# Kernel tuning notes

Measured on AMD Instinct MI355X. Metric: run time of the kernel, lower is better.

Reference implementation:

```python
import jax, jax.numpy as jnp
import numpy as np

ALPHA = 0.2  # LeakyReLU negative slope
NEG_INF = -9e15  # mask value used by the torch dense GAT layer

def _gat_layer(x, adj, W, a1, a2):
    # x: [N, F], W: [F, Fh], a1/a2: [Fh]
    Wh = x @ W                                   # [N, Fh]
    f1 = Wh @ a1                                 # [N] source scores
    f2 = Wh @ a2                                 # [N] dest scores
    e = jax.nn.leaky_relu(f1[:, None] + f2[None, :], ALPHA)  # [N, N]
    att = jnp.where(adj > 0, e, NEG_INF)
    att = jax.nn.softmax(att, axis=1)
    return att @ Wh                              # [N, Fh]

def setup_inputs():
    key = jax.random.key(0)
    ks = jax.random.split(key, 8)
    N, F, H, Fh, C = 6144, 512, 4, 64, 40
    x = jax.random.normal(ks[0], (N, F), jnp.float32)
    # sparse-ish binary adjacency with self loops (dense storage as in the module)
    adj = (jax.random.uniform(ks[1], (N, N)) < 0.005).astype(jnp.float32)
    adj = jnp.maximum(adj, jnp.eye(N, dtype=jnp.float32))
    s = 1.0 / np.sqrt(Fh)
    W = jax.random.normal(ks[2], (H, F, Fh), jnp.float32) * s
    a1 = jax.random.normal(ks[3], (H, Fh), jnp.float32) * s
    a2 = jax.random.normal(ks[4], (H, Fh), jnp.float32) * s
    so = 1.0 / np.sqrt(C)
    Wo = jax.random.normal(ks[5], (H * Fh, C), jnp.float32) * so
    ao1 = jax.random.normal(ks[6], (C,), jnp.float32) * so
    ao2 = jax.random.normal(ks[7], (C,), jnp.float32) * so
    return {"x": x, "adj": adj, "W": W, "a1": a1, "a2": a2,
            "Wo": Wo, "ao1": ao1, "ao2": ao2}

def reference(x, adj, W, a1, a2, Wo, ao1, ao2):
    N = x.shape[0]
    # multi-head layer (concat=True -> ELU applied inside each head)
    heads = jax.vmap(_gat_layer, in_axes=(None, None, 0, 0, 0))(x, adj, W, a1, a2)  # [H, N, Fh]
    h = jax.nn.elu(heads)
    h = jnp.transpose(h, (1, 0, 2)).reshape(N, -1)   # concat heads -> [N, H*Fh]
    # output attention layer (concat=False), then outer ELU from GAT.forward
    out = jax.nn.elu(_gat_layer(h, adj, Wo, ao1, ao2))  # [N, C]
    return jax.nn.log_softmax(out, axis=1)
```

## Files before the change

### kernel.cpp

```cpp
#include <hip/hip_runtime.h>
#include <stdint.h>

#define N_NODES 6144
#define F_IN 512
#define NHEAD 4
#define FH 64
#define HF 256
#define NCLS 40
#define NCLSP 48
#define CAP 192
#define LRELU_ALPHA 0.2f

typedef __bf16 bf16x8 __attribute__((ext_vector_type(8)));
typedef float floatx4 __attribute__((ext_vector_type(4)));

__device__ __forceinline__ float b2f(uint16_t u){
    union { float f; uint32_t i; } x; x.i = ((uint32_t)u) << 16; return x.f;
}
__device__ __forceinline__ uint16_t f2b(float f){
    union { float f; uint32_t i; } x; x.f = f;
    uint32_t r = x.i + 0x7FFFu + ((x.i >> 16) & 1u);
    return (uint16_t)(r >> 16);
}


__global__ void k_prep(const float* __restrict__ x, const float* __restrict__ W,
                       const float* __restrict__ Wo,
                       uint16_t* __restrict__ xh, uint16_t* __restrict__ xl,
                       uint16_t* __restrict__ Wth, uint16_t* __restrict__ Wtl,
                       uint16_t* __restrict__ Woth, uint16_t* __restrict__ Wotl){
    int b = blockIdx.x, t = threadIdx.x;
    if (b < 1536){
        int T = b * 256 + t;
        int n = T >> 6, q8 = T & 63;
        const float4* xp = reinterpret_cast<const float4*>(x + (size_t)n * F_IN + q8 * 8);
        float4 v0 = xp[0], v1 = xp[1];
        int rt = n >> 4, m = n & 15, kc = q8 >> 2, q = q8 & 3;
        size_t off = ((size_t)(rt * 16 + kc) << 9) + (q * 16 + m) * 8;
        ushort4 h0, h1, l0, l1;
        h0.x = f2b(v0.x); l0.x = f2b(v0.x - b2f(h0.x));
        h0.y = f2b(v0.y); l0.y = f2b(v0.y - b2f(h0.y));
        h0.z = f2b(v0.z); l0.z = f2b(v0.z - b2f(h0.z));
        h0.w = f2b(v0.w); l0.w = f2b(v0.w - b2f(h0.w));
        h1.x = f2b(v1.x); l1.x = f2b(v1.x - b2f(h1.x));
        h1.y = f2b(v1.y); l1.y = f2b(v1.y - b2f(h1.y));
        h1.z = f2b(v1.z); l1.z = f2b(v1.z - b2f(h1.z));
        h1.w = f2b(v1.w); l1.w = f2b(v1.w - b2f(h1.w));
        *reinterpret_cast<ushort4*>(xh + off)     = h0;
        *reinterpret_cast<ushort4*>(xh + off + 4) = h1;
        *reinterpret_cast<ushort4*>(xl + off)     = l0;
        *reinterpret_cast<ushort4*>(xl + off + 4) = l1;
    } else if (b < 1600){
        int T = (b - 1536) * 256 + t;
        int c = T >> 6, q8 = T & 63;
        int h = c >> 6, f = c & 63, k0 = q8 * 8;
        int rt = c >> 4, m = c & 15, kc = q8 >> 2, q = q8 & 3;
        size_t off = ((size_t)(rt * 16 + kc) << 9) + (q * 16 + m) * 8;
        #pragma unroll
        for (int j = 0; j < 8; j++){
            float v = W[h * 32768 + (k0 + j) * 64 + f];
            uint16_t hi = f2b(v);
            Wth[off + j] = hi;
            Wtl[off + j] = f2b(v - b2f(hi));
        }
    } else {
        int T = (b - 1600) * 256 + t;
        int c = T >> 8, k = T & 255;
        float v = (c < NCLS) ? Wo[k * NCLS + c] : 0.f;
        uint16_t hi = f2b(v);
        Woth[c * HF + k] = hi;
        Wotl[c * HF + k] = f2b(v - b2f(hi));
    }
}

__global__ void k_build_csr(const float* __restrict__ adj, int* __restrict__ cnt,
                            int* __restrict__ idxbuf){
    __shared__ int scnt;
    int i = blockIdx.x, t = threadIdx.x;
    if (t == 0) scnt = 0;
    __syncthreads();
    const float4* row = reinterpret_cast<const float4*>(adj + (size_t)i * N_NODES);
    int* out = idxbuf + (size_t)i * CAP;
    for (int q = t; q < N_NODES / 4; q += 256){
        float4 v = row[q];
        int j0 = q * 4;
        if (v.x != 0.f){ int p = atomicAdd(&scnt, 1); if (p < CAP) out[p] = j0;     }
        if (v.y != 0.f){ int p = atomicAdd(&scnt, 1); if (p < CAP) out[p] = j0 + 1; }
        if (v.z != 0.f){ int p = atomicAdd(&scnt, 1); if (p < CAP) out[p] = j0 + 2; }
        if (v.w != 0.f){ int p = atomicAdd(&scnt, 1); if (p < CAP) out[p] = j0 + 3; }
    }
    __syncthreads();
    if (t == 0) cnt[i] = scnt < CAP ? scnt : CAP;
}

__global__ void k_gemm1(const uint16_t* __restrict__ xh, const uint16_t* __restrict__ xl,
                        const uint16_t* __restrict__ Wth, const uint16_t* __restrict__ Wtl,
                        float* __restrict__ Wh1){
    int w = threadIdx.x >> 6, l = threadIdx.x & 63;
    int rt0 = blockIdx.x * 4 + (w & 1) * 2;
    int ct0 = blockIdx.y * 4 + (w >> 1) * 2;
    const uint16_t* pah = xh  + ((size_t)rt0 << 13) + l * 8;
    const uint16_t* pal = xl  + ((size_t)rt0 << 13) + l * 8;
    const uint16_t* pbh = Wth + ((size_t)ct0 << 13) + l * 8;
    const uint16_t* pbl = Wtl + ((size_t)ct0 << 13) + l * 8;
    floatx4 acc[2][2] = {};
    for (int kc = 0; kc < 16; kc++){
        int o0 = kc * 512, o1 = kc * 512 + 8192;
        bf16x8 a0h = *reinterpret_cast<const bf16x8*>(pah + o0);
        bf16x8 a0l = *reinterpret_cast<const bf16x8*>(pal + o0);
        bf16x8 a1h = *reinterpret_cast<const bf16x8*>(pah + o1);
        bf16x8 a1l = *reinterpret_cast<const bf16x8*>(pal + o1);
        bf16x8 b0h = *reinterpret_cast<const bf16x8*>(pbh + o0);
        bf16x8 b0l = *reinterpret_cast<const bf16x8*>(pbl + o0);
        bf16x8 b1h = *reinterpret_cast<const bf16x8*>(pbh + o1);
        bf16x8 b1l = *reinterpret_cast<const bf16x8*>(pbl + o1);
        acc[0][0] = __builtin_amdgcn_mfma_f32_16x16x32_bf16(a0h, b0l, acc[0][0], 0, 0, 0);
        acc[0][0] = __builtin_amdgcn_mfma_f32_16x16x32_bf16(a0l, b0h, acc[0][0], 0, 0, 0);
        acc[0][0] = __builtin_amdgcn_mfma_f32_16x16x32_bf16(a0h, b0h, acc[0][0], 0, 0, 0);
        acc[0][1] = __builtin_amdgcn_mfma_f32_16x16x32_bf16(a0h, b1l, acc[0][1], 0, 0, 0);
        acc[0][1] = __builtin_amdgcn_mfma_f32_16x16x32_bf16(a0l, b1h, acc[0][1], 0, 0, 0);
        acc[0][1] = __builtin_amdgcn_mfma_f32_16x16x32_bf16(a0h, b1h, acc[0][1], 0, 0, 0);
        acc[1][0] = __builtin_amdgcn_mfma_f32_16x16x32_bf16(a1h, b0l, acc[1][0], 0, 0, 0);
        acc[1][0] = __builtin_amdgcn_mfma_f32_16x16x32_bf16(a1l, b0h, acc[1][0], 0, 0, 0);
        acc[1][0] = __builtin_amdgcn_mfma_f32_16x16x32_bf16(a1h, b0h, acc[1][0], 0, 0, 0);
        acc[1][1] = __builtin_amdgcn_mfma_f32_16x16x32_bf16(a1h, b1l, acc[1][1], 0, 0, 0);
        acc[1][1] = __builtin_amdgcn_mfma_f32_16x16x32_bf16(a1l, b1h, acc[1][1], 0, 0, 0);
        acc[1][1] = __builtin_amdgcn_mfma_f32_16x16x32_bf16(a1h, b1h, acc[1][1], 0, 0, 0);
    }
    int m = l & 15, q = l >> 4;
    #pragma unroll
    for (int fr = 0; fr < 2; fr++){
        #pragma unroll
        for (int fc = 0; fc < 2; fc++){
            int col  = (ct0 + fc) * 16 + m;
            int rowb = (rt0 + fr) * 16 + q * 4;
            #pragma unroll
            for (int r = 0; r < 4; r++)
                Wh1[(size_t)(rowb + r) * HF + col] = acc[fr][fc][r];
        }
    }
}

__global__ void k_f12(const float* __restrict__ Wh1, const float* __restrict__ a1,
                      const float* __restrict__ a2, float* __restrict__ f1,
                      float* __restrict__ f2){
    int n = blockIdx.x;
    int h = threadIdx.x >> 6, l = threadIdx.x & 63;
    float w = Wh1[(size_t)n * HF + h * FH + l];
    float s1 = w * a1[h * FH + l];
    float s2 = w * a2[h * FH + l];
    for (int off = 32; off; off >>= 1){
        s1 += __shfl_xor(s1, off);
        s2 += __shfl_xor(s2, off);
    }
    if (l == 0){ f1[h * N_NODES + n] = s1; f2[h * N_NODES + n] = s2; }
}

__global__ void k_attn1(const int* __restrict__ cnt, const int* __restrict__ idxbuf,
                        const float* __restrict__ Wh1, const float* __restrict__ f1,
                        const float* __restrict__ f2,
                        uint16_t* __restrict__ hch, uint16_t* __restrict__ hcl){
    int i = blockIdx.x, h = threadIdx.x >> 6, l = threadIdx.x & 63;
    int c = cnt[i];
    __shared__ int   sidx[CAP];
    __shared__ float sp[NHEAD][CAP];
    const int* src = idxbuf + (size_t)i * CAP;
    for (int e = threadIdx.x; e < c; e += 256) sidx[e] = src[e];
    __syncthreads();
    float f1i = f1[h * N_NODES + i];
    const float* f2h = f2 + h * N_NODES;
    float mx = -1e30f;
    for (int e = l; e < c; e += 64){
        float s = f1i + f2h[sidx[e]];
        s = s > 0.f ? s : LRELU_ALPHA * s;
        sp[h][e] = s;
        mx = fmaxf(mx, s);
    }
    for (int off = 32; off; off >>= 1) mx = fmaxf(mx, __shfl_xor(mx, off));
    float ssum = 0.f;
    for (int e = l; e < c; e += 64){
        float p = __expf(sp[h][e] - mx);
        sp[h][e] = p;
        ssum += p;
    }
    for (int off = 32; off; off >>= 1) ssum += __shfl_xor(ssum, off);
    float inv = 1.f / ssum;
    float acc = 0.f;
    const float* whb = Wh1 + h * FH + l;
    int e = 0;
    for (; e + 4 <= c; e += 4){
        int j0 = sidx[e], j1 = sidx[e+1], j2 = sidx[e+2], j3 = sidx[e+3];
        float v0 = whb[(size_t)j0 * HF];
        float v1 = whb[(size_t)j1 * HF];
        float v2 = whb[(size_t)j2 * HF];
        float v3 = whb[(size_t)j3 * HF];
        acc += sp[h][e]*v0 + sp[h][e+1]*v1 + sp[h][e+2]*v2 + sp[h][e+3]*v3;
    }
    for (; e < c; e++)
        acc += sp[h][e] * whb[(size_t)sidx[e] * HF];
    acc *= inv;
    float v = acc > 0.f ? acc : __expf(acc) - 1.f;
    uint16_t hi = f2b(v);
    uint16_t lo = f2b(v - b2f(hi));
    size_t o = (size_t)i * HF + h * FH + l;
    hch[o] = hi;
    hcl[o] = lo;
}

__global__ void k_gemm2(const uint16_t* __restrict__ hch, const uint16_t* __restrict__ hcl,
                        const uint16_t* __restrict__ Woth, const uint16_t* __restrict__ Wotl,
                        float* __restrict__ Wh2){
    int w = threadIdx.x >> 6, l = threadIdx.x & 63;
    int r0 = blockIdx.x * 32 + w * 16;
    int c0 = blockIdx.y * 16;
    int m = l & 15, q = l >> 4;
    const uint16_t* pah = hch  + (size_t)(r0 + m) * HF + q * 8;
    const uint16_t* pal = hcl  + (size_t)(r0 + m) * HF + q * 8;
    const uint16_t* pbh = Woth + (size_t)(c0 + m) * HF + q * 8;
    const uint16_t* pbl = Wotl + (size_t)(c0 + m) * HF + q * 8;
    floatx4 acc = {};
    for (int k0 = 0; k0 < HF; k0 += 32){
        bf16x8 ah = *reinterpret_cast<const bf16x8*>(pah + k0);
        bf16x8 al = *reinterpret_cast<const bf16x8*>(pal + k0);
        bf16x8 bh = *reinterpret_cast<const bf16x8*>(pbh + k0);
        bf16x8 bl = *reinterpret_cast<const bf16x8*>(pbl + k0);
        acc = __builtin_amdgcn_mfma_f32_16x16x32_bf16(ah, bl, acc, 0, 0, 0);
        acc = __builtin_amdgcn_mfma_f32_16x16x32_bf16(al, bh, acc, 0, 0, 0);
        acc = __builtin_amdgcn_mfma_f32_16x16x32_bf16(ah, bh, acc, 0, 0, 0);
    }
    int col = c0 + m;
    if (col < NCLS){
        int rowb = r0 + q * 4;
        #pragma unroll
        for (int r = 0; r < 4; r++)
            Wh2[(size_t)(rowb + r) * NCLS + col] = acc[r];
    }
}

__global__ void k_f12o(const float* __restrict__ Wh2, const float* __restrict__ ao1,
                       const float* __restrict__ ao2, float* __restrict__ f1o,
                       float* __restrict__ f2o){
    int w = threadIdx.x >> 6, l = threadIdx.x & 63;
    int n = blockIdx.x * 4 + w;
    float t1 = 0.f, t2 = 0.f;
    if (l < NCLS){
        float v = Wh2[(size_t)n * NCLS + l];
        t1 = v * ao1[l];
        t2 = v * ao2[l];
    }
    for (int off = 32; off; off >>= 1){
        t1 += __shfl_xor(t1, off);
        t2 += __shfl_xor(t2, off);
    }
    if (l == 0){ f1o[n] = t1; f2o[n] = t2; }
}

__global__ void k_attn2(const int* __restrict__ cnt, const int* __restrict__ idxbuf,
                        const float* __restrict__ Wh2, const float* __restrict__ f1o,
                        const float* __restrict__ f2o, float* __restrict__ out){
    int i = blockIdx.x, l = threadIdx.x;
    int c = cnt[i];
    __shared__ int   sidx[CAP];
    __shared__ float sp[CAP];
    const int* src = idxbuf + (size_t)i * CAP;
    for (int e = l; e < c; e += 64) sidx[e] = src[e];
    __syncthreads();
    float f1i = f1o[i];
    float mx = -1e30f;
    for (int e = l; e < c; e += 64){
        float s = f1i + f2o[sidx[e]];
        s = s > 0.f ? s : LRELU_ALPHA * s;
        sp[e] = s;
        mx = fmaxf(mx, s);
    }
    for (int off = 32; off; off >>= 1) mx = fmaxf(mx, __shfl_xor(mx, off));
    __syncthreads();
    float ssum = 0.f;
    for (int e = l; e < c; e += 64){
        float p = __expf(sp[e] - mx);
        sp[e] = p;
        ssum += p;
    }
    for (int off = 32; off; off >>= 1) ssum += __shfl_xor(ssum, off);
    float inv = 1.f / ssum;
    __syncthreads();
    float acc = 0.f;
    if (l < NCLS){
        const float* wb = Wh2 + l;
        int e = 0;
        for (; e + 4 <= c; e += 4){
            int j0 = sidx[e], j1 = sidx[e+1], j2 = sidx[e+2], j3 = sidx[e+3];
            float v0 = wb[(size_t)j0 * NCLS];
            float v1 = wb[(size_t)j1 * NCLS];
            float v2 = wb[(size_t)j2 * NCLS];
            float v3 = wb[(size_t)j3 * NCLS];
            acc += sp[e]*v0 + sp[e+1]*v1 + sp[e+2]*v2 + sp[e+3]*v3;
        }
        for (; e < c; e++)
            acc += sp[e] * wb[(size_t)sidx[e] * NCLS];
        acc *= inv;
    }
    float o = (l < NCLS) ? (acc > 0.f ? acc : __expf(acc) - 1.f) : -1e30f;
    float m2 = o;
    for (int off = 32; off; off >>= 1) m2 = fmaxf(m2, __shfl_xor(m2, off));
    float ex = (l < NCLS) ? __expf(o - m2) : 0.f;
    for (int off = 32; off; off >>= 1) ex += __shfl_xor(ex, off);
    float res = o - m2 - logf(ex);
    if (l < NCLS) out[(size_t)i * NCLS + l] = res;
}

extern "C" void kernel_launch(void* const* d_in, const int* in_sizes, int n_in,
                              void* d_out, int out_size, void* d_ws, size_t ws_size,
                              hipStream_t stream) {
    const float* x   = (const float*)d_in[0];
    const float* adj = (const float*)d_in[1];
    const float* W   = (const float*)d_in[2];
    const float* a1  = (const float*)d_in[3];
    const float* a2  = (const float*)d_in[4];
    const float* Wo  = (const float*)d_in[5];
    const float* ao1 = (const float*)d_in[6];
    const float* ao2 = (const float*)d_in[7];
    float* out = (float*)d_out;

    char* ws = (char*)d_ws;
    int*      nbr_cnt = (int*)     (ws + 0);
    int*      nbr_idx = (int*)     (ws + 24576);
    uint16_t* xh      = (uint16_t*)(ws + 4743168);
    uint16_t* xl      = (uint16_t*)(ws + 11034624);
    uint16_t* Wth     = (uint16_t*)(ws + 17326080);
    uint16_t* Wtl     = (uint16_t*)(ws + 17588224);
    uint16_t* Woth    = (uint16_t*)(ws + 17850368);
    uint16_t* Wotl    = (uint16_t*)(ws + 17874944);
    float*    Wh1     = (float*)   (ws + 17899520);
    float*    f1      = (float*)   (ws + 24190976);
    float*    f2      = (float*)   (ws + 24289280);
    uint16_t* hch     = (uint16_t*)(ws + 24387584);
    uint16_t* hcl     = (uint16_t*)(ws + 27533312);
    float*    Wh2     = (float*)   (ws + 30679040);
    float*    f1o     = (float*)   (ws + 31662080);
    float*    f2o     = (float*)   (ws + 31686656);

    hipLaunchKernelGGL(k_prep,      dim3(1648),    dim3(256), 0, stream, x, W, Wo, xh, xl, Wth, Wtl, Woth, Wotl);
    hipLaunchKernelGGL(k_build_csr, dim3(6144),    dim3(256), 0, stream, adj, nbr_cnt, nbr_idx);
    hipLaunchKernelGGL(k_gemm1,     dim3(96, 4),   dim3(256), 0, stream, xh, xl, Wth, Wtl, Wh1);
    hipLaunchKernelGGL(k_f12,       dim3(6144),    dim3(256), 0, stream, Wh1, a1, a2, f1, f2);
    hipLaunchKernelGGL(k_attn1,     dim3(6144),    dim3(256), 0, stream, nbr_cnt, nbr_idx, Wh1, f1, f2, hch, hcl);
    hipLaunchKernelGGL(k_gemm2,     dim3(192, 3),  dim3(128), 0, stream, hch, hcl, Woth, Wotl, Wh2);
    hipLaunchKernelGGL(k_f12o,      dim3(1536),    dim3(256), 0, stream, Wh2, ao1, ao2, f1o, f2o);
    hipLaunchKernelGGL(k_attn2,     dim3(6144),    dim3(64),  0, stream, nbr_cnt, nbr_idx, Wh2, f1o, f2o, out);
}
```

Measured before the change: 299.4 us.

## Fuse x split-conversion and f1/f2 scores into GEMM1, merge CSR with prep

The separate x-to-bf16 hi/lo prepass goes away: the GEMM1 kernel now loads fp32 x directly and splits it in registers. The f1/f2 attention-score kernel is folded into the GEMM1 epilogue using shuffle and shared-memory reductions. CSR construction is merged into the weight-prep launch, and Wh1 is stored as bf16 to halve gather traffic in attn1. The aim is to cut launches and the large x intermediate round-trip, at the cost of less accurate Wh1 values in aggregation and redundant per-block conversion of x.

```diff
diff --git a/kernel.cpp b/kernel.cpp
--- a/kernel.cpp
+++ b/kernel.cpp
@@ -7,12 +7,12 @@
 #define FH 64
 #define HF 256
 #define NCLS 40
-#define NCLSP 48
 #define CAP 192
 #define LRELU_ALPHA 0.2f
 
 typedef __bf16 bf16x8 __attribute__((ext_vector_type(8)));
 typedef float floatx4 __attribute__((ext_vector_type(4)));
+typedef uint16_t u16x8 __attribute__((ext_vector_type(8)));
 
 __device__ __forceinline__ float b2f(uint16_t u){
     union { float f; uint32_t i; } x; x.i = ((uint32_t)u) << 16; return x.f;
@@ -22,36 +22,43 @@
     uint32_t r = x.i + 0x7FFFu + ((x.i >> 16) & 1u);
     return (uint16_t)(r >> 16);
 }
-
-
-__global__ void k_prep(const float* __restrict__ x, const float* __restrict__ W,
-                       const float* __restrict__ Wo,
-                       uint16_t* __restrict__ xh, uint16_t* __restrict__ xl,
-                       uint16_t* __restrict__ Wth, uint16_t* __restrict__ Wtl,
-                       uint16_t* __restrict__ Woth, uint16_t* __restrict__ Wotl){
+__device__ __forceinline__ void cvt_split8(const float* __restrict__ s, bf16x8& hv, bf16x8& lv){
+    union { u16x8 u; bf16x8 b; } H, L;
+    #pragma unroll
+    for (int j = 0; j < 8; j++){
+        uint16_t hb = f2b(s[j]);
+        H.u[j] = hb;
+        L.u[j] = f2b(s[j] - b2f(hb));
+    }
+    hv = H.b; lv = L.b;
+}
+
+
+__global__ void k_csr_prep(const float* __restrict__ adj, const float* __restrict__ W,
+                           const float* __restrict__ Wo,
+                           int* __restrict__ cnt, int* __restrict__ idxbuf,
+                           uint16_t* __restrict__ Wth, uint16_t* __restrict__ Wtl,
+                           uint16_t* __restrict__ Woth, uint16_t* __restrict__ Wotl){
+    __shared__ int scnt;
     int b = blockIdx.x, t = threadIdx.x;
-    if (b < 1536){
-        int T = b * 256 + t;
-        int n = T >> 6, q8 = T & 63;
-        const float4* xp = reinterpret_cast<const float4*>(x + (size_t)n * F_IN + q8 * 8);
-        float4 v0 = xp[0], v1 = xp[1];
-        int rt = n >> 4, m = n & 15, kc = q8 >> 2, q = q8 & 3;
-        size_t off = ((size_t)(rt * 16 + kc) << 9) + (q * 16 + m) * 8;
-        ushort4 h0, h1, l0, l1;
-        h0.x = f2b(v0.x); l0.x = f2b(v0.x - b2f(h0.x));
-        h0.y = f2b(v0.y); l0.y = f2b(v0.y - b2f(h0.y));
-        h0.z = f2b(v0.z); l0.z = f2b(v0.z - b2f(h0.z));
-        h0.w = f2b(v0.w); l0.w = f2b(v0.w - b2f(h0.w));
-        h1.x = f2b(v1.x); l1.x = f2b(v1.x - b2f(h1.x));
-        h1.y = f2b(v1.y); l1.y = f2b(v1.y - b2f(h1.y));
-        h1.z = f2b(v1.z); l1.z = f2b(v1.z - b2f(h1.z));
-        h1.w = f2b(v1.w); l1.w = f2b(v1.w - b2f(h1.w));
-        *reinterpret_cast<ushort4*>(xh + off)     = h0;
-        *reinterpret_cast<ushort4*>(xh + off + 4) = h1;
-        *reinterpret_cast<ushort4*>(xl + off)     = l0;
-        *reinterpret_cast<ushort4*>(xl + off + 4) = l1;
-    } else if (b < 1600){
-        int T = (b - 1536) * 256 + t;
+    if (b < N_NODES){
+        int i = b;
+        if (t == 0) scnt = 0;
+        __syncthreads();
+        const float4* row = reinterpret_cast<const float4*>(adj + (size_t)i * N_NODES);
+        int* out = idxbuf + (size_t)i * CAP;
+        for (int q = t; q < N_NODES / 4; q += 256){
+            float4 v = row[q];
+            int j0 = q * 4;
+            if (v.x != 0.f){ int p = atomicAdd(&scnt, 1); if (p < CAP) out[p] = j0;     }
+            if (v.y != 0.f){ int p = atomicAdd(&scnt, 1); if (p < CAP) out[p] = j0 + 1; }
+            if (v.z != 0.f){ int p = atomicAdd(&scnt, 1); if (p < CAP) out[p] = j0 + 2; }
+            if (v.w != 0.f){ int p = atomicAdd(&scnt, 1); if (p < CAP) out[p] = j0 + 3; }
+        }
+        __syncthreads();
+        if (t == 0) cnt[i] = scnt < CAP ? scnt : CAP;
+    } else if (b < N_NODES + 64){
+        int T = (b - N_NODES) * 256 + t;
         int c = T >> 6, q8 = T & 63;
         int h = c >> 6, f = c & 63, k0 = q8 * 8;
         int rt = c >> 4, m = c & 15, kc = q8 >> 2, q = q8 & 3;
@@ -64,7 +71,7 @@
             Wtl[off + j] = f2b(v - b2f(hi));
         }
     } else {
-        int T = (b - 1600) * 256 + t;
+        int T = (b - N_NODES - 64) * 256 + t;
         int c = T >> 8, k = T & 255;
         float v = (c < NCLS) ? Wo[k * NCLS + c] : 0.f;
         uint16_t hi = f2b(v);
@@ -73,91 +80,93 @@
     }
 }
 
-__global__ void k_build_csr(const float* __restrict__ adj, int* __restrict__ cnt,
-                            int* __restrict__ idxbuf){
-    __shared__ int scnt;
-    int i = blockIdx.x, t = threadIdx.x;
-    if (t == 0) scnt = 0;
-    __syncthreads();
-    const float4* row = reinterpret_cast<const float4*>(adj + (size_t)i * N_NODES);
-    int* out = idxbuf + (size_t)i * CAP;
-    for (int q = t; q < N_NODES / 4; q += 256){
-        float4 v = row[q];
-        int j0 = q * 4;
-        if (v.x != 0.f){ int p = atomicAdd(&scnt, 1); if (p < CAP) out[p] = j0;     }
-        if (v.y != 0.f){ int p = atomicAdd(&scnt, 1); if (p < CAP) out[p] = j0 + 1; }
-        if (v.z != 0.f){ int p = atomicAdd(&scnt, 1); if (p < CAP) out[p] = j0 + 2; }
-        if (v.w != 0.f){ int p = atomicAdd(&scnt, 1); if (p < CAP) out[p] = j0 + 3; }
-    }
-    __syncthreads();
-    if (t == 0) cnt[i] = scnt < CAP ? scnt : CAP;
-}
-
-__global__ void k_gemm1(const uint16_t* __restrict__ xh, const uint16_t* __restrict__ xl,
+__global__ void k_gemm1(const float* __restrict__ x,
                         const uint16_t* __restrict__ Wth, const uint16_t* __restrict__ Wtl,
-                        float* __restrict__ Wh1){
+                        const float* __restrict__ a1, const float* __restrict__ a2,
+                        uint16_t* __restrict__ Wh1b, float* __restrict__ f1,
+                        float* __restrict__ f2){
+    __shared__ float sred[2][2][64];
     int w = threadIdx.x >> 6, l = threadIdx.x & 63;
-    int rt0 = blockIdx.x * 4 + (w & 1) * 2;
-    int ct0 = blockIdx.y * 4 + (w >> 1) * 2;
-    const uint16_t* pah = xh  + ((size_t)rt0 << 13) + l * 8;
-    const uint16_t* pal = xl  + ((size_t)rt0 << 13) + l * 8;
-    const uint16_t* pbh = Wth + ((size_t)ct0 << 13) + l * 8;
-    const uint16_t* pbl = Wtl + ((size_t)ct0 << 13) + l * 8;
+    int h = blockIdx.y, bx = blockIdx.x;
+    int m = l & 15, q = l >> 4;
+    int rt0 = bx * 4 + (w & 1) * 2;
+    int ctl = (w >> 1) * 2;
+    const float* pa0 = x + (size_t)(rt0 * 16 + m) * F_IN + q * 8;
+    const float* pa1 = pa0 + 16 * F_IN;
+    const uint16_t* pb0h = Wth + ((size_t)(h * 4 + ctl) << 13) + l * 8;
+    const uint16_t* pb0l = Wtl + ((size_t)(h * 4 + ctl) << 13) + l * 8;
+    const uint16_t* pb1h = pb0h + 8192;
+    const uint16_t* pb1l = pb0l + 8192;
     floatx4 acc[2][2] = {};
     for (int kc = 0; kc < 16; kc++){
-        int o0 = kc * 512, o1 = kc * 512 + 8192;
-        bf16x8 a0h = *reinterpret_cast<const bf16x8*>(pah + o0);
-        bf16x8 a0l = *reinterpret_cast<const bf16x8*>(pal + o0);
-        bf16x8 a1h = *reinterpret_cast<const bf16x8*>(pah + o1);
-        bf16x8 a1l = *reinterpret_cast<const bf16x8*>(pal + o1);
-        bf16x8 b0h = *reinterpret_cast<const bf16x8*>(pbh + o0);
-        bf16x8 b0l = *reinterpret_cast<const bf16x8*>(pbl + o0);
-        bf16x8 b1h = *reinterpret_cast<const bf16x8*>(pbh + o1);
-        bf16x8 b1l = *reinterpret_cast<const bf16x8*>(pbl + o1);
+        float av0[8], av1[8];
+        *reinterpret_cast<float4*>(av0)     = *reinterpret_cast<const float4*>(pa0 + kc * 32);
+        *reinterpret_cast<float4*>(av0 + 4) = *reinterpret_cast<const float4*>(pa0 + kc * 32 + 4);
+        *reinterpret_cast<float4*>(av1)     = *reinterpret_cast<const float4*>(pa1 + kc * 32);
+        *reinterpret_cast<float4*>(av1 + 4) = *reinterpret_cast<const float4*>(pa1 + kc * 32 + 4);
+        bf16x8 b0h = *reinterpret_cast<const bf16x8*>(pb0h + kc * 512);
+        bf16x8 b0l = *reinterpret_cast<const bf16x8*>(pb0l + kc * 512);
+        bf16x8 b1h = *reinterpret_cast<const bf16x8*>(pb1h + kc * 512);
+        bf16x8 b1l = *reinterpret_cast<const bf16x8*>(pb1l + kc * 512);
+        bf16x8 a0h, a0l, a1h_, a1l_;
+        cvt_split8(av0, a0h, a0l);
+        cvt_split8(av1, a1h_, a1l_);
         acc[0][0] = __builtin_amdgcn_mfma_f32_16x16x32_bf16(a0h, b0l, acc[0][0], 0, 0, 0);
         acc[0][0] = __builtin_amdgcn_mfma_f32_16x16x32_bf16(a0l, b0h, acc[0][0], 0, 0, 0);
         acc[0][0] = __builtin_amdgcn_mfma_f32_16x16x32_bf16(a0h, b0h, acc[0][0], 0, 0, 0);
         acc[0][1] = __builtin_amdgcn_mfma_f32_16x16x32_bf16(a0h, b1l, acc[0][1], 0, 0, 0);
         acc[0][1] = __builtin_amdgcn_mfma_f32_16x16x32_bf16(a0l, b1h, acc[0][1], 0, 0, 0);
         acc[0][1] = __builtin_amdgcn_mfma_f32_16x16x32_bf16(a0h, b1h, acc[0][1], 0, 0, 0);
-        acc[1][0] = __builtin_amdgcn_mfma_f32_16x16x32_bf16(a1h, b0l, acc[1][0], 0, 0, 0);
-        acc[1][0] = __builtin_amdgcn_mfma_f32_16x16x32_bf16(a1l, b0h, acc[1][0], 0, 0, 0);
-        acc[1][0] = __builtin_amdgcn_mfma_f32_16x16x32_bf16(a1h, b0h, acc[1][0], 0, 0, 0);
-        acc[1][1] = __builtin_amdgcn_mfma_f32_16x16x32_bf16(a1h, b1l, acc[1][1], 0, 0, 0);
-        acc[1][1] = __builtin_amdgcn_mfma_f32_16x16x32_bf16(a1l, b1h, acc[1][1], 0, 0, 0);
-        acc[1][1] = __builtin_amdgcn_mfma_f32_16x16x32_bf16(a1h, b1h, acc[1][1], 0, 0, 0);
-    }
-    int m = l & 15, q = l >> 4;
+        acc[1][0] = __builtin_amdgcn_mfma_f32_16x16x32_bf16(a1h_, b0l, acc[1][0], 0, 0, 0);
+        acc[1][0] = __builtin_amdgcn_mfma_f32_16x16x32_bf16(a1l_, b0h, acc[1][0], 0, 0, 0);
+        acc[1][0] = __builtin_amdgcn_mfma_f32_16x16x32_bf16(a1h_, b0h, acc[1][0], 0, 0, 0);
+        acc[1][1] = __builtin_amdgcn_mfma_f32_16x16x32_bf16(a1h_, b1l, acc[1][1], 0, 0, 0);
+        acc[1][1] = __builtin_amdgcn_mfma_f32_16x16x32_bf16(a1l_, b1h, acc[1][1], 0, 0, 0);
+        acc[1][1] = __builtin_amdgcn_mfma_f32_16x16x32_bf16(a1h_, b1h, acc[1][1], 0, 0, 0);
+    }
     #pragma unroll
     for (int fr = 0; fr < 2; fr++){
         #pragma unroll
         for (int fc = 0; fc < 2; fc++){
-            int col  = (ct0 + fc) * 16 + m;
+            int col = h * 64 + (ctl + fc) * 16 + m;
             int rowb = (rt0 + fr) * 16 + q * 4;
             #pragma unroll
             for (int r = 0; r < 4; r++)
-                Wh1[(size_t)(rowb + r) * HF + col] = acc[fr][fc][r];
-        }
-    }
-}
-
-__global__ void k_f12(const float* __restrict__ Wh1, const float* __restrict__ a1,
-                      const float* __restrict__ a2, float* __restrict__ f1,
-                      float* __restrict__ f2){
-    int n = blockIdx.x;
-    int h = threadIdx.x >> 6, l = threadIdx.x & 63;
-    float w = Wh1[(size_t)n * HF + h * FH + l];
-    float s1 = w * a1[h * FH + l];
-    float s2 = w * a2[h * FH + l];
-    for (int off = 32; off; off >>= 1){
-        s1 += __shfl_xor(s1, off);
-        s2 += __shfl_xor(s2, off);
-    }
-    if (l == 0){ f1[h * N_NODES + n] = s1; f2[h * N_NODES + n] = s2; }
+                Wh1b[(size_t)(rowb + r) * HF + col] = f2b(acc[fr][fc][r]);
+        }
+    }
+    float a1v0 = a1[h * FH + (ctl + 0) * 16 + m];
+    float a1v1 = a1[h * FH + (ctl + 1) * 16 + m];
+    float a2v0 = a2[h * FH + (ctl + 0) * 16 + m];
+    float a2v1 = a2[h * FH + (ctl + 1) * 16 + m];
+    #pragma unroll
+    for (int fr = 0; fr < 2; fr++){
+        #pragma unroll
+        for (int r = 0; r < 4; r++){
+            float s1 = acc[fr][0][r] * a1v0 + acc[fr][1][r] * a1v1;
+            float s2 = acc[fr][0][r] * a2v0 + acc[fr][1][r] * a2v1;
+            #pragma unroll
+            for (int off = 1; off < 16; off <<= 1){
+                s1 += __shfl_xor(s1, off);
+                s2 += __shfl_xor(s2, off);
+            }
+            if (m == 0){
+                int lr = ((w & 1) * 2 + fr) * 16 + q * 4 + r;
+                sred[w >> 1][0][lr] = s1;
+                sred[w >> 1][1][lr] = s2;
+            }
+        }
+    }
+    __syncthreads();
+    if (threadIdx.x < 64){
+        int n = bx * 64 + threadIdx.x;
+        f1[h * N_NODES + n] = sred[0][0][threadIdx.x] + sred[1][0][threadIdx.x];
+        f2[h * N_NODES + n] = sred[0][1][threadIdx.x] + sred[1][1][threadIdx.x];
+    }
 }
 
 __global__ void k_attn1(const int* __restrict__ cnt, const int* __restrict__ idxbuf,
-                        const float* __restrict__ Wh1, const float* __restrict__ f1,
+                        const uint16_t* __restrict__ Wh1b, const float* __restrict__ f1,
                         const float* __restrict__ f2,
                         uint16_t* __restrict__ hch, uint16_t* __restrict__ hcl){
     int i = blockIdx.x, h = threadIdx.x >> 6, l = threadIdx.x & 63;
@@ -186,18 +195,18 @@
     for (int off = 32; off; off >>= 1) ssum += __shfl_xor(ssum, off);
     float inv = 1.f / ssum;
     float acc = 0.f;
-    const float* whb = Wh1 + h * FH + l;
+    const uint16_t* whb = Wh1b + h * FH + l;
     int e = 0;
     for (; e + 4 <= c; e += 4){
         int j0 = sidx[e], j1 = sidx[e+1], j2 = sidx[e+2], j3 = sidx[e+3];
-        float v0 = whb[(size_t)j0 * HF];
-        float v1 = whb[(size_t)j1 * HF];
-        float v2 = whb[(size_t)j2 * HF];
-        float v3 = whb[(size_t)j3 * HF];
+        float v0 = b2f(whb[(size_t)j0 * HF]);
+        float v1 = b2f(whb[(size_t)j1 * HF]);
+        float v2 = b2f(whb[(size_t)j2 * HF]);
+        float v3 = b2f(whb[(size_t)j3 * HF]);
         acc += sp[h][e]*v0 + sp[h][e+1]*v1 + sp[h][e+2]*v2 + sp[h][e+3]*v3;
     }
     for (; e < c; e++)
-        acc += sp[h][e] * whb[(size_t)sidx[e] * HF];
+        acc += sp[h][e] * b2f(whb[(size_t)sidx[e] * HF]);
     acc *= inv;
     float v = acc > 0.f ? acc : __expf(acc) - 1.f;
     uint16_t hi = f2b(v);
@@ -325,27 +334,27 @@
     char* ws = (char*)d_ws;
     int*      nbr_cnt = (int*)     (ws + 0);
     int*      nbr_idx = (int*)     (ws + 24576);
-    uint16_t* xh      = (uint16_t*)(ws + 4743168);
-    uint16_t* xl      = (uint16_t*)(ws + 11034624);
-    uint16_t* Wth     = (uint16_t*)(ws + 17326080);
-    uint16_t* Wtl     = (uint16_t*)(ws + 17588224);
-    uint16_t* Woth    = (uint16_t*)(ws + 17850368);
-    uint16_t* Wotl    = (uint16_t*)(ws + 17874944);
-    float*    Wh1     = (float*)   (ws + 17899520);
-    float*    f1      = (float*)   (ws + 24190976);
-    float*    f2      = (float*)   (ws + 24289280);
-    uint16_t* hch     = (uint16_t*)(ws + 24387584);
-    uint16_t* hcl     = (uint16_t*)(ws + 27533312);
-    float*    Wh2     = (float*)   (ws + 30679040);
-    float*    f1o     = (float*)   (ws + 31662080);
-    float*    f2o     = (float*)   (ws + 31686656);
-
-    hipLaunchKernelGGL(k_prep,      dim3(1648),    dim3(256), 0, stream, x, W, Wo, xh, xl, Wth, Wtl, Woth, Wotl);
-    hipLaunchKernelGGL(k_build_csr, dim3(6144),    dim3(256), 0, stream, adj, nbr_cnt, nbr_idx);
-    hipLaunchKernelGGL(k_gemm1,     dim3(96, 4),   dim3(256), 0, stream, xh, xl, Wth, Wtl, Wh1);
-    hipLaunchKernelGGL(k_f12,       dim3(6144),    dim3(256), 0, stream, Wh1, a1, a2, f1, f2);
-    hipLaunchKernelGGL(k_attn1,     dim3(6144),    dim3(256), 0, stream, nbr_cnt, nbr_idx, Wh1, f1, f2, hch, hcl);
-    hipLaunchKernelGGL(k_gemm2,     dim3(192, 3),  dim3(128), 0, stream, hch, hcl, Woth, Wotl, Wh2);
-    hipLaunchKernelGGL(k_f12o,      dim3(1536),    dim3(256), 0, stream, Wh2, ao1, ao2, f1o, f2o);
-    hipLaunchKernelGGL(k_attn2,     dim3(6144),    dim3(64),  0, stream, nbr_cnt, nbr_idx, Wh2, f1o, f2o, out);
-}
+    uint16_t* Wth     = (uint16_t*)(ws + 4743168);
+    uint16_t* Wtl     = (uint16_t*)(ws + 5005312);
+    uint16_t* Woth    = (uint16_t*)(ws + 5267456);
+    uint16_t* Wotl    = (uint16_t*)(ws + 5292032);
+    uint16_t* Wh1b    = (uint16_t*)(ws + 5316608);
+    float*    f1      = (float*)   (ws + 8462336);
+    float*    f2      = (float*)   (ws + 8560640);
+    uint16_t* hch     = (uint16_t*)(ws + 8658944);
+    uint16_t* hcl     = (uint16_t*)(ws + 11804672);
+    float*    Wh2     = (float*)   (ws + 14950400);
+    float*    f1o     = (float*)   (ws + 15933440);
+    float*    f2o     = (float*)   (ws + 15958016);
+
+    hipLaunchKernelGGL(k_csr_prep, dim3(6256),   dim3(256), 0, stream, adj, W, Wo,
+                       nbr_cnt, nbr_idx, Wth, Wtl, Woth, Wotl);
+    hipLaunchKernelGGL(k_gemm1,    dim3(96, 4),  dim3(256), 0, stream, x, Wth, Wtl,
+                       a1, a2, Wh1b, f1, f2);
+    hipLaunchKernelGGL(k_attn1,    dim3(6144),   dim3(256), 0, stream, nbr_cnt, nbr_idx,
+                       Wh1b, f1, f2, hch, hcl);
+    hipLaunchKernelGGL(k_gemm2,    dim3(192, 3), dim3(128), 0, stream, hch, hcl, Woth, Wotl, Wh2);
+    hipLaunchKernelGGL(k_f12o,     dim3(1536),   dim3(256), 0, stream, Wh2, ao1, ao2, f1o, f2o);
+    hipLaunchKernelGGL(k_attn2,    dim3(6144),   dim3(64),  0, stream, nbr_cnt, nbr_idx,
+                       Wh2, f1o, f2o, out);
+}
```

Result: faster. 287.7 us (-3.9%).
